# Optimization experiments

Hardware: AMD Instinct MI355X
Metric: run time of the kernel (lower is better)

Reference implementation:

```python
import jax, jax.numpy as jnp
import numpy as np

OUT = 7   # output_size
SR = 2    # sampling_ratio


def _roi_align(feat_bhwc, rois, batch_idx, sx, sy):
    """RoIAlign (torchvision semantics, aligned=False) with per-axis spatial scale.
    feat_bhwc: [B,H,W,C]; rois: [K,4] (x1,y1,x2,y2) in padded-image coords;
    batch_idx: [K] int32; returns [K,C,OUT,OUT]."""
    B, H, W, C = feat_bhwc.shape
    K = rois.shape[0]
    x1 = rois[:, 0] * sx
    y1 = rois[:, 1] * sy
    x2 = rois[:, 2] * sx
    y2 = rois[:, 3] * sy
    bw = jnp.maximum(x2 - x1, 1.0) / OUT   # bin width  [K]
    bh = jnp.maximum(y2 - y1, 1.0) / OUT   # bin height [K]
    # sample position j in [0, OUT*SR): offset (j+0.5)/SR bins from roi start
    g = (jnp.arange(OUT * SR, dtype=feat_bhwc.dtype) + 0.5) / SR
    ys = y1[:, None] + g[None, :] * bh[:, None]   # [K, P] with P = OUT*SR
    xs = x1[:, None] + g[None, :] * bw[:, None]   # [K, P]
    Y = ys[:, :, None]                            # [K,P,1]
    X = xs[:, None, :]                            # [K,1,P]
    valid = (Y >= -1.0) & (Y <= H) & (X >= -1.0) & (X <= W)  # [K,P,P]
    Yc = jnp.clip(Y, 0.0, H - 1)
    Xc = jnp.clip(X, 0.0, W - 1)
    y0f = jnp.floor(Yc)
    x0f = jnp.floor(Xc)
    ly = Yc - y0f
    lx = Xc - x0f
    hy = 1.0 - ly
    hx = 1.0 - lx
    y0i = y0f.astype(jnp.int32)
    x0i = x0f.astype(jnp.int32)
    y1i = jnp.minimum(y0i + 1, H - 1)
    x1i = jnp.minimum(x0i + 1, W - 1)
    b = batch_idx[:, None, None]                  # [K,1,1]

    def gat(yi, xi):
        # broadcasts indices to [K,P,P]; gathers [K,P,P,C]
        return feat_bhwc[b, yi, xi]

    out = ((hy * hx)[..., None] * gat(y0i, x0i)
           + (hy * lx)[..., None] * gat(y0i, x1i)
           + (ly * hx)[..., None] * gat(y1i, x0i)
           + (ly * lx)[..., None] * gat(y1i, x1i))
    out = out * valid[..., None].astype(out.dtype)
    # average SRxSR samples per output bin
    out = out.reshape(K, OUT, SR, OUT, SR, C).mean(axis=(2, 4))
    return out.transpose(0, 3, 1, 2)  # [K,C,OUT,OUT]


def reference(x0, x1, x2, boxes, ratio, offset, shape):
    B, C0, H0, W0 = x0.shape
    # bilinear upsample (half-pixel centers == torch align_corners=False) and concat
    up1 = jax.image.resize(x1, (B, x1.shape[1], H0, W0), method='bilinear')
    up2 = jax.image.resize(x2, (B, x2.shape[1], H0, W0), method='bilinear')
    feat = jnp.concatenate([x0, up1, up2], axis=1)      # [B, 3*C, H0, W0]
    feat_bhwc = feat.transpose(0, 2, 3, 1)
    # map boxes from original-image coords to padded/resized coords
    rH, rW = ratio[:, 0], ratio[:, 1]
    top, left = offset[:, 0], offset[:, 1]
    mul = jnp.stack([rW, rH, rW, rH], axis=-1)[:, None, :]   # [B,1,4]
    add = jnp.stack([left, top, left, top], axis=-1)[:, None, :]
    rois = (boxes * mul + add).reshape(-1, 4)                # [K,4]
    N = boxes.shape[1]
    batch_idx = jnp.repeat(jnp.arange(B, dtype=jnp.int32), N)
    # per-axis spatial scale from the first meta (as in the torch code)
    padded_h = jnp.floor(shape[0, 0] * rH[0] + 2.0 * top[0])
    padded_w = jnp.floor(shape[0, 1] * rW[0] + 2.0 * left[0])
    sx = W0 / padded_w
    sy = H0 / padded_h
    return _roi_align(feat_bhwc, rois, batch_idx, sx, sy)   # [B*N, 3*C, 7, 7]


def setup_inputs():
    key = jax.random.key(0)
    k = jax.random.split(key, 5)
    B, C, N = 2, 256, 128
    IH, IW = 800.0, 1216.0  # original image size; stride-8 top level -> 100x152
    x0 = jax.random.normal(k[0], (B, C, 100, 152), jnp.float32)
    x1 = jax.random.normal(k[1], (B, C, 50, 76), jnp.float32)
    x2 = jax.random.normal(k[2], (B, C, 25, 38), jnp.float32)
    xy = jax.random.uniform(k[3], (B, N, 2)) * jnp.array([IW - 64.0, IH - 64.0], jnp.float32)
    wh = 16.0 + jax.random.uniform(k[4], (B, N, 2)) * 200.0
    boxes = jnp.concatenate([xy, jnp.minimum(xy + wh, jnp.array([IW, IH], jnp.float32))], axis=-1)
    ratio = jnp.ones((B, 2), jnp.float32)
    offset = jnp.zeros((B, 2), jnp.float32)
    shape = jnp.tile(jnp.array([[IH, IW]], jnp.float32), (B, 1))
    return dict(x0=x0, x1=x1, x2=x2, boxes=boxes, ratio=ratio, offset=offset, shape=shape)
```

## Files before the change

### kernel.cpp

```cpp
#include <hip/hip_runtime.h>
#include <hip/hip_bf16.h>

constexpr int B  = 2;
constexpr int C  = 256;
constexpr int H0 = 100, W0 = 152;
constexpr int H1 = 50,  W1 = 76;
constexpr int H2 = 25,  W2 = 38;
constexpr int N  = 128;
constexpr int K  = B * N;
constexpr int CT = 3 * C;
constexpr int OUTS = 7;

#define DEV __device__ __forceinline__

DEV float ldbf(const __hip_bfloat16* p) { return __bfloat162float(*p); }

DEV void st8bf(__hip_bfloat16* p, const float* v) {
  union { __hip_bfloat16 h[8]; uint4 u; } pk;
  #pragma unroll
  for (int j = 0; j < 8; ++j) pk.h[j] = __float2bfloat16(v[j]);
  *reinterpret_cast<uint4*>(p) = pk.u;
}

DEV void unp(uint32_t u, float& lo, float& hi) {
  lo = __uint_as_float(u << 16);
  hi = __uint_as_float(u & 0xffff0000u);
}

__global__ __launch_bounds__(256) void fuse_kernel(
    const float* __restrict__ x0, const float* __restrict__ x1,
    const float* __restrict__ x2, __hip_bfloat16* __restrict__ feat) {
  __shared__ float buf[64 * 153];
  const int blk  = blockIdx.x;
  const int tile = blk % 12;
  const int by   = blk / 12;
  const int y    = by % H0;
  const int b    = by / H0;
  const int t    = threadIdx.x;
  const int level = tile >> 2;
  const int c0l   = (tile & 3) * 64;

  __hip_bfloat16* const orow =
      feat + (((size_t)b * H0 + y) * W0) * CT + tile * 64;

  if (level == 0) {
    const float* src = x0 + (((size_t)b * C + c0l) * H0 + y) * W0;
    for (int i = 0; i < 10; ++i) {
      const int lin = i * 256 + t;
      if (lin < 64 * 38) {
        const int cl = lin / 38, xq = lin % 38;
        const float4 v =
            *reinterpret_cast<const float4*>(src + (size_t)cl * (H0 * W0) + xq * 4);
        float* d = &buf[cl * 153 + xq * 4];
        d[0] = v.x; d[1] = v.y; d[2] = v.z; d[3] = v.w;
      }
    }
    __syncthreads();
    for (int i = 0; i < 5; ++i) {
      const int lin = i * 256 + t;
      if (lin < 1216) {
        const int x = lin >> 3, cq = lin & 7;
        float v[8];
        #pragma unroll
        for (int j = 0; j < 8; ++j) v[j] = buf[(cq * 8 + j) * 153 + x];
        st8bf(orow + (size_t)x * CT + cq * 8, v);
      }
    }
  } else if (level == 1) {
    const float fy = fminf(fmaxf(y * 0.5f - 0.25f, 0.f), (float)(H1 - 1));
    const int   y0i = (int)fy;
    const float ly  = fy - (float)y0i;
    const int   y1i = min(y0i + 1, H1 - 1);
    const int rstep = (y1i - y0i) * W1;
    const float* s0 = x1 + (((size_t)b * C + c0l) * H1 + y0i) * W1;
    for (int i = 0; i < 5; ++i) {
      const int lin = i * 256 + t;
      if (lin < 64 * 19) {
        const int cl = lin / 19, xq = lin % 19;
        const float* p = s0 + (size_t)cl * (H1 * W1) + xq * 4;
        const float4 v0 = *reinterpret_cast<const float4*>(p);
        const float4 v1 = *reinterpret_cast<const float4*>(p + rstep);
        float* d = &buf[cl * 81 + xq * 4];
        d[0] = v0.x + ly * (v1.x - v0.x);
        d[1] = v0.y + ly * (v1.y - v0.y);
        d[2] = v0.z + ly * (v1.z - v0.z);
        d[3] = v0.w + ly * (v1.w - v0.w);
      }
    }
    __syncthreads();
    for (int i = 0; i < 5; ++i) {
      const int lin = i * 256 + t;
      if (lin < 1216) {
        const int x = lin >> 3, cq = lin & 7;
        const float fx = fminf(fmaxf(x * 0.5f - 0.25f, 0.f), (float)(W1 - 1));
        const int   x0i = (int)fx;
        const float lx  = fx - (float)x0i;
        const int   x1i = min(x0i + 1, W1 - 1);
        const float* r = &buf[cq * 8 * 81];
        float v[8];
        #pragma unroll
        for (int j = 0; j < 8; ++j) {
          const float a = r[j * 81 + x0i], bb = r[j * 81 + x1i];
          v[j] = a + lx * (bb - a);
        }
        st8bf(orow + (size_t)x * CT + cq * 8, v);
      }
    }
  } else {
    const float fy = fminf(fmaxf(y * 0.25f - 0.375f, 0.f), (float)(H2 - 1));
    const int   y0i = (int)fy;
    const float ly  = fy - (float)y0i;
    const int   y1i = min(y0i + 1, H2 - 1);
    const int rstep = (y1i - y0i) * W2;
    const float* s0 = x2 + (((size_t)b * C + c0l) * H2 + y0i) * W2;
    for (int i = 0; i < 5; ++i) {
      const int lin = i * 256 + t;
      if (lin < 64 * 19) {
        const int cl = lin / 19, xq = lin % 19;
        const float* p = s0 + (size_t)cl * (H2 * W2) + xq * 2;
        const float2 v0 = *reinterpret_cast<const float2*>(p);
        const float2 v1 = *reinterpret_cast<const float2*>(p + rstep);
        float* d = &buf[cl * 39 + xq * 2];
        d[0] = v0.x + ly * (v1.x - v0.x);
        d[1] = v0.y + ly * (v1.y - v0.y);
      }
    }
    __syncthreads();
    for (int i = 0; i < 5; ++i) {
      const int lin = i * 256 + t;
      if (lin < 1216) {
        const int x = lin >> 3, cq = lin & 7;
        const float fx = fminf(fmaxf(x * 0.25f - 0.375f, 0.f), (float)(W2 - 1));
        const int   x0i = (int)fx;
        const float lx  = fx - (float)x0i;
        const int   x1i = min(x0i + 1, W2 - 1);
        const float* r = &buf[cq * 8 * 39];
        float v[8];
        #pragma unroll
        for (int j = 0; j < 8; ++j) {
          const float a = r[j * 39 + x0i], bb = r[j * 39 + x1i];
          v[j] = a + lx * (bb - a);
        }
        st8bf(orow + (size_t)x * CT + cq * 8, v);
      }
    }
  }
}

__global__ __launch_bounds__(192) void roi_kernel(
    const __hip_bfloat16* __restrict__ feat, const float* __restrict__ boxes,
    const float* __restrict__ ratio, const float* __restrict__ offset,
    const float* __restrict__ shape, float* __restrict__ out) {
  __shared__ float lds[384 * 49];
  const int blk = blockIdx.x;
  const int cg  = blk & 1;
  const int k   = blk >> 1;
  const int b   = k >> 7;
  const int t   = threadIdx.x;
  const int c0  = cg * 384 + 2 * t;

  const float padded_h = floorf(shape[0] * ratio[0] + 2.f * offset[0]);
  const float padded_w = floorf(shape[1] * ratio[1] + 2.f * offset[1]);
  const float sx = (float)W0 / padded_w;
  const float sy = (float)H0 / padded_h;
  const float rHb = ratio[b * 2 + 0], rWb = ratio[b * 2 + 1];
  const float topb = offset[b * 2 + 0], leftb = offset[b * 2 + 1];
  const float* bx = boxes + (size_t)k * 4;
  const float x1s = (bx[0] * rWb + leftb) * sx;
  const float y1s = (bx[1] * rHb + topb) * sy;
  const float x2s = (bx[2] * rWb + leftb) * sx;
  const float y2s = (bx[3] * rHb + topb) * sy;
  const float bw = fmaxf(x2s - x1s, 1.f) / OUTS;
  const float bh = fmaxf(y2s - y1s, 1.f) / OUTS;

  float hx[14], lx[14];
  int xo0[14], xo1[14];
  #pragma unroll
  for (int s = 0; s < 14; ++s) {
    const float X = x1s + ((float)s * 0.5f + 0.25f) * bw;
    const bool vx = (X >= -1.f) && (X <= (float)W0);
    const float Xc = fminf(fmaxf(X, 0.f), (float)(W0 - 1));
    const float xf = floorf(Xc);
    const float l  = Xc - xf;
    const int x0i = (int)xf;
    const int x1i = min(x0i + 1, W0 - 1);
    hx[s]  = vx ? (1.f - l) : 0.f;
    lx[s]  = vx ? l : 0.f;
    xo0[s] = x0i * (CT / 2);
    xo1[s] = x1i * (CT / 2);
  }

  const uint32_t* fb = reinterpret_cast<const uint32_t*>(
      feat + (size_t)b * (H0 * W0 * CT) + c0);

  for (int ph = 0; ph < OUTS; ++ph) {
    float accL[OUTS] = {0.f, 0.f, 0.f, 0.f, 0.f, 0.f, 0.f};
    float accH[OUTS] = {0.f, 0.f, 0.f, 0.f, 0.f, 0.f, 0.f};
    #pragma unroll
    for (int iy = 0; iy < 2; ++iy) {
      const float Y = y1s + ((float)ph + (float)iy * 0.5f + 0.25f) * bh;
      const bool vy = (Y >= -1.f) && (Y <= (float)H0);
      const float Yc = fminf(fmaxf(Y, 0.f), (float)(H0 - 1));
      const float yf = floorf(Yc);
      const float ly = Yc - yf;
      const int y0i = (int)yf;
      const int y1i = min(y0i + 1, H0 - 1);
      const float w0 = vy ? (1.f - ly) * 0.25f : 0.f;
      const float w1 = vy ? ly * 0.25f : 0.f;
      const uint32_t* r0 = fb + (size_t)y0i * (W0 * CT / 2);
      const uint32_t* r1 = fb + (size_t)y1i * (W0 * CT / 2);
      uint32_t v00[14], v01[14], v10[14], v11[14];
      #pragma unroll
      for (int s = 0; s < 14; ++s) {
        v00[s] = r0[xo0[s]];
        v01[s] = r0[xo1[s]];
        v10[s] = r1[xo0[s]];
        v11[s] = r1[xo1[s]];
      }
      #pragma unroll
      for (int s = 0; s < 14; ++s) {
        float a00l, a00h, a01l, a01h, a10l, a10h, a11l, a11h;
        unp(v00[s], a00l, a00h);
        unp(v01[s], a01l, a01h);
        unp(v10[s], a10l, a10h);
        unp(v11[s], a11l, a11h);
        accL[s >> 1] += w0 * (hx[s] * a00l + lx[s] * a01l) +
                        w1 * (hx[s] * a10l + lx[s] * a11l);
        accH[s >> 1] += w0 * (hx[s] * a00h + lx[s] * a01h) +
                        w1 * (hx[s] * a10h + lx[s] * a11h);
      }
    }
    #pragma unroll
    for (int pw = 0; pw < OUTS; ++pw) {
      lds[(2 * t + 0) * 49 + ph * 7 + pw] = accL[pw];
      lds[(2 * t + 1) * 49 + ph * 7 + pw] = accH[pw];
    }
  }
  __syncthreads();
  float* ob = out + (size_t)k * (CT * 49) + (size_t)cg * (384 * 49);
  const float4* ls = reinterpret_cast<const float4*>(lds);
  float4* os = reinterpret_cast<float4*>(ob);
  for (int i = 0; i < 25; ++i) {
    const int idx = i * 192 + t;
    if (idx < 4704) os[idx] = ls[idx];
  }
}

extern "C" void kernel_launch(void* const* d_in, const int* in_sizes, int n_in,
                              void* d_out, int out_size, void* d_ws, size_t ws_size,
                              hipStream_t stream) {
  const float* x0     = (const float*)d_in[0];
  const float* x1     = (const float*)d_in[1];
  const float* x2     = (const float*)d_in[2];
  const float* boxes  = (const float*)d_in[3];
  const float* ratio  = (const float*)d_in[4];
  const float* offset = (const float*)d_in[5];
  const float* shape  = (const float*)d_in[6];
  float* out = (float*)d_out;

  __hip_bfloat16* feat = (__hip_bfloat16*)d_ws;

  fuse_kernel<<<dim3(B * H0 * 12), dim3(256), 0, stream>>>(x0, x1, x2, feat);
  roi_kernel<<<dim3(K * 2), dim3(192), 0, stream>>>(feat, boxes, ratio,
                                                    offset, shape, out);
}
```

Before: 142.8 us.

## Split ROI kernel by output-row halves with one channel per thread

```diff
diff --git a/kernel.cpp b/kernel.cpp
--- a/kernel.cpp
+++ b/kernel.cpp
@@ -20,11 +20,6 @@
   #pragma unroll
   for (int j = 0; j < 8; ++j) pk.h[j] = __float2bfloat16(v[j]);
   *reinterpret_cast<uint4*>(p) = pk.u;
-}
-
-DEV void unp(uint32_t u, float& lo, float& hi) {
-  lo = __uint_as_float(u << 16);
-  hi = __uint_as_float(u & 0xffff0000u);
 }
 
 __global__ __launch_bounds__(256) void fuse_kernel(
@@ -147,17 +142,60 @@
   }
 }
 
-__global__ __launch_bounds__(192) void roi_kernel(
+template <int PH0, int NPH>
+DEV void roi_body(const __hip_bfloat16* __restrict__ fb, float y1s, float bh,
+                  const float (&hx)[14], const float (&lx)[14],
+                  const int (&xo0)[14], const int (&xo1)[14],
+                  float* __restrict__ op) {
+  float acc[NPH][7];
+  #pragma unroll
+  for (int i = 0; i < NPH; ++i)
+    #pragma unroll
+    for (int j = 0; j < 7; ++j) acc[i][j] = 0.f;
+
+  #pragma unroll
+  for (int pi = 0; pi < NPH; ++pi) {
+    const int ph = PH0 + pi;
+    #pragma unroll
+    for (int iy = 0; iy < 2; ++iy) {
+      const float Y = y1s + ((float)ph + (float)iy * 0.5f + 0.25f) * bh;
+      const bool vy = (Y >= -1.f) && (Y <= (float)H0);
+      const float Yc = fminf(fmaxf(Y, 0.f), (float)(H0 - 1));
+      const float yf = floorf(Yc);
+      const float ly = Yc - yf;
+      const int y0i = (int)yf;
+      const int y1i = min(y0i + 1, H0 - 1);
+      const float w0 = vy ? (1.f - ly) * 0.25f : 0.f;
+      const float w1 = vy ? ly * 0.25f : 0.f;
+      const __hip_bfloat16* r0 = fb + (size_t)y0i * (W0 * CT);
+      const __hip_bfloat16* r1 = fb + (size_t)y1i * (W0 * CT);
+      #pragma unroll
+      for (int s = 0; s < 14; ++s) {
+        const float a00 = ldbf(r0 + xo0[s]);
+        const float a01 = ldbf(r0 + xo1[s]);
+        const float a10 = ldbf(r1 + xo0[s]);
+        const float a11 = ldbf(r1 + xo1[s]);
+        acc[pi][s >> 1] += w0 * (hx[s] * a00 + lx[s] * a01) +
+                           w1 * (hx[s] * a10 + lx[s] * a11);
+      }
+    }
+  }
+  #pragma unroll
+  for (int i = 0; i < NPH * 7; ++i) op[i] = acc[i / 7][i % 7];
+}
+
+__global__ __launch_bounds__(256, 4) void roi_kernel(
     const __hip_bfloat16* __restrict__ feat, const float* __restrict__ boxes,
     const float* __restrict__ ratio, const float* __restrict__ offset,
     const float* __restrict__ shape, float* __restrict__ out) {
-  __shared__ float lds[384 * 49];
   const int blk = blockIdx.x;
-  const int cg  = blk & 1;
-  const int k   = blk >> 1;
+  const int phh = blk / 768;
+  const int r   = blk - phh * 768;
+  const int cg  = r % 3;
+  const int k   = r / 3;
   const int b   = k >> 7;
   const int t   = threadIdx.x;
-  const int c0  = cg * 384 + 2 * t;
+  const int c   = cg * 256 + t;
 
   const float padded_h = floorf(shape[0] * ratio[0] + 2.f * offset[0]);
   const float padded_w = floorf(shape[1] * ratio[1] + 2.f * offset[1]);
@@ -186,63 +224,17 @@
     const int x1i = min(x0i + 1, W0 - 1);
     hx[s]  = vx ? (1.f - l) : 0.f;
     lx[s]  = vx ? l : 0.f;
-    xo0[s] = x0i * (CT / 2);
-    xo1[s] = x1i * (CT / 2);
-  }
-
-  const uint32_t* fb = reinterpret_cast<const uint32_t*>(
-      feat + (size_t)b * (H0 * W0 * CT) + c0);
-
-  for (int ph = 0; ph < OUTS; ++ph) {
-    float accL[OUTS] = {0.f, 0.f, 0.f, 0.f, 0.f, 0.f, 0.f};
-    float accH[OUTS] = {0.f, 0.f, 0.f, 0.f, 0.f, 0.f, 0.f};
-    #pragma unroll
-    for (int iy = 0; iy < 2; ++iy) {
-      const float Y = y1s + ((float)ph + (float)iy * 0.5f + 0.25f) * bh;
-      const bool vy = (Y >= -1.f) && (Y <= (float)H0);
-      const float Yc = fminf(fmaxf(Y, 0.f), (float)(H0 - 1));
-      const float yf = floorf(Yc);
-      const float ly = Yc - yf;
-      const int y0i = (int)yf;
-      const int y1i = min(y0i + 1, H0 - 1);
-      const float w0 = vy ? (1.f - ly) * 0.25f : 0.f;
-      const float w1 = vy ? ly * 0.25f : 0.f;
-      const uint32_t* r0 = fb + (size_t)y0i * (W0 * CT / 2);
-      const uint32_t* r1 = fb + (size_t)y1i * (W0 * CT / 2);
-      uint32_t v00[14], v01[14], v10[14], v11[14];
-      #pragma unroll
-      for (int s = 0; s < 14; ++s) {
-        v00[s] = r0[xo0[s]];
-        v01[s] = r0[xo1[s]];
-        v10[s] = r1[xo0[s]];
-        v11[s] = r1[xo1[s]];
-      }
-      #pragma unroll
-      for (int s = 0; s < 14; ++s) {
-        float a00l, a00h, a01l, a01h, a10l, a10h, a11l, a11h;
-        unp(v00[s], a00l, a00h);
-        unp(v01[s], a01l, a01h);
-        unp(v10[s], a10l, a10h);
-        unp(v11[s], a11l, a11h);
-        accL[s >> 1] += w0 * (hx[s] * a00l + lx[s] * a01l) +
-                        w1 * (hx[s] * a10l + lx[s] * a11l);
-        accH[s >> 1] += w0 * (hx[s] * a00h + lx[s] * a01h) +
-                        w1 * (hx[s] * a10h + lx[s] * a11h);
-      }
-    }
-    #pragma unroll
-    for (int pw = 0; pw < OUTS; ++pw) {
-      lds[(2 * t + 0) * 49 + ph * 7 + pw] = accL[pw];
-      lds[(2 * t + 1) * 49 + ph * 7 + pw] = accH[pw];
-    }
-  }
-  __syncthreads();
-  float* ob = out + (size_t)k * (CT * 49) + (size_t)cg * (384 * 49);
-  const float4* ls = reinterpret_cast<const float4*>(lds);
-  float4* os = reinterpret_cast<float4*>(ob);
-  for (int i = 0; i < 25; ++i) {
-    const int idx = i * 192 + t;
-    if (idx < 4704) os[idx] = ls[idx];
+    xo0[s] = x0i * CT;
+    xo1[s] = x1i * CT;
+  }
+
+  const __hip_bfloat16* fb = feat + (size_t)b * (H0 * W0 * CT) + c;
+  float* op = out + (size_t)k * (CT * 49) + (size_t)c * 49 + phh * 28;
+
+  if (phh == 0) {
+    roi_body<0, 4>(fb, y1s, bh, hx, lx, xo0, xo1, op);
+  } else {
+    roi_body<4, 3>(fb, y1s, bh, hx, lx, xo0, xo1, op);
   }
 }
 
@@ -261,6 +253,6 @@
   __hip_bfloat16* feat = (__hip_bfloat16*)d_ws;
 
   fuse_kernel<<<dim3(B * H0 * 12), dim3(256), 0, stream>>>(x0, x1, x2, feat);
-  roi_kernel<<<dim3(K * 2), dim3(192), 0, stream>>>(feat, boxes, ratio,
-                                                    offset, shape, out);
-}
+  roi_kernel<<<dim3(1536), dim3(256), 0, stream>>>(feat, boxes, ratio,
+                                                   offset, shape, out);
+}
```

Result: slower. 202.7 us (+42.0%).
